# Performance work log

Measured on AMD Instinct MI355X. Metric: run time of the kernel, lower is better.

Reference implementation:

```python
import jax, jax.numpy as jnp
import numpy as np

N_NODES = 100000
N_EDGES = 1600000
IN_DIM = 128
HID_DIM = 64
OUT_DIM = 1


def setup_inputs() -> dict:
    key = jax.random.key(0)
    k = jax.random.split(key, 8)
    x = jax.random.normal(k[0], (N_NODES, IN_DIM), dtype=jnp.float32)
    edge_index = jax.random.randint(k[1], (2, N_EDGES), 0, N_NODES, dtype=jnp.int64)
    # GCNConv layer 1: weight [IN, HID], bias [HID] (glorot-ish scale)
    W1 = jax.random.normal(k[2], (IN_DIM, HID_DIM), dtype=jnp.float32) / np.sqrt(IN_DIM)
    b1 = jnp.zeros((HID_DIM,), dtype=jnp.float32)
    W2 = jax.random.normal(k[3], (HID_DIM, HID_DIM), dtype=jnp.float32) / np.sqrt(HID_DIM)
    b2 = jnp.zeros((HID_DIM,), dtype=jnp.float32)
    Wfc = jax.random.normal(k[4], (HID_DIM, OUT_DIM), dtype=jnp.float32) / np.sqrt(HID_DIM)
    bfc = jnp.zeros((OUT_DIM,), dtype=jnp.float32)
    return {"x": x, "edge_index": edge_index, "W1": W1, "b1": b1,
            "W2": W2, "b2": b2, "Wfc": Wfc, "bfc": bfc}


def _gcn_norm(edge_index, n_nodes):
    # PyG GCNConv default: add self-loops, symmetric normalization.
    src, dst = edge_index[0], edge_index[1]
    loop = jnp.arange(n_nodes, dtype=src.dtype)
    src = jnp.concatenate([src, loop])
    dst = jnp.concatenate([dst, loop])
    deg = jax.ops.segment_sum(jnp.ones_like(dst, dtype=jnp.float32), dst,
                              num_segments=n_nodes)
    deg_isqrt = jax.lax.rsqrt(deg)  # deg >= 1 thanks to self-loops
    norm = deg_isqrt[src] * deg_isqrt[dst]  # [E+N]
    return src, dst, norm


def _gcn_conv(x, src, dst, norm, W, b, n_nodes):
    h = x @ W                      # [N, D_out] dense transform first (D_out <= D_in)
    msg = h[src] * norm[:, None]   # gather + normalize  [E+N, D_out]
    out = jax.ops.segment_sum(msg, dst, num_segments=n_nodes)  # scatter-add
    return out + b


def reference(x, edge_index, W1, b1, W2, b2, Wfc, bfc):
    n = x.shape[0]
    src, dst, norm = _gcn_norm(edge_index, n)
    h = jax.nn.relu(_gcn_conv(x, src, dst, norm, W1, b1, n))
    h = jax.nn.relu(_gcn_conv(h, src, dst, norm, W2, b2, n))
    return h @ Wfc + bfc  # [N, 1]
```

## Files before the change

kernel.cpp:

```cpp
#include <hip/hip_runtime.h>


#define IN_DIM 128
#define HID 64
#define B1 256
#define MAXNC 512
#define BCAP 8192

typedef unsigned int uint;
typedef unsigned short ushort;
typedef __attribute__((ext_vector_type(8))) short short8;
typedef __attribute__((ext_vector_type(4))) float f32x4;

__device__ inline uint pack_bf16x2(float a, float b) {
    uint ua = __builtin_bit_cast(uint, a);
    uint ub = __builtin_bit_cast(uint, b);
    ua += 0x7fffu + ((ua >> 16) & 1u);
    ub += 0x7fffu + ((ub >> 16) & 1u);
    return (ua >> 16) | (ub & 0xffff0000u);
}
__device__ inline float bf_lo(uint g) { return __builtin_bit_cast(float, g << 16); }
__device__ inline float bf_hi(uint g) { return __builtin_bit_cast(float, g & 0xffff0000u); }
__device__ inline uint rne_hi_bits(float a) {
    uint u = __builtin_bit_cast(uint, a);
    return (u + 0x7fffu + ((u >> 16) & 1u)) & 0xffff0000u;
}
__device__ inline float bitf(uint u) { return __builtin_bit_cast(float, u); }

__global__ __launch_bounds__(512) void scatter_bkt(
        const int* __restrict__ src, const int* __restrict__ dst,
        int* __restrict__ bktcnt, uint* __restrict__ slack,
        int E, int NC, int chunk,
        const float* __restrict__ W1f, const float* __restrict__ W2f,
        ushort* __restrict__ w1h, ushort* __restrict__ w1l,
        ushort* __restrict__ w2h, ushort* __restrict__ w2l) {
    int t = threadIdx.x, blk = blockIdx.x;
    if (blk < B1) {
        __shared__ int h[MAXNC], cur[MAXNC];
        for (int i = t; i < NC; i += 512) h[i] = 0;
        __syncthreads();
        int s = blk * chunk, e = min(E, s + chunk);
        for (int i = s + t; i < e; i += 512) atomicAdd(&h[dst[i] >> 8], 1);
        __syncthreads();
        for (int i = t; i < NC; i += 512)
            cur[i] = h[i] ? atomicAdd(&bktcnt[i], h[i]) : 0;
        __syncthreads();
        for (int i = s + t; i < e; i += 512) {
            int d = dst[i], b = d >> 8;
            int p = atomicAdd(&cur[b], 1);
            slack[(size_t)b * BCAP + p] = ((uint)src[i] << 8) | (uint)(d & 255);
        }
    } else if (blk == B1) {
        for (int i = t; i < 128 * 64; i += 512) {
            int k = i >> 6, c = i & 63;
            float v = W1f[i];
            uint rh = rne_hi_bits(v);
            w1h[c * 128 + k] = (ushort)(rh >> 16);
            w1l[c * 128 + k] = (ushort)(rne_hi_bits(v - bitf(rh)) >> 16);
        }
    } else {
        for (int i = t; i < 64 * 64; i += 512) {
            int k = i >> 6, c = i & 63;
            float v = W2f[i];
            uint rh = rne_hi_bits(v);
            w2h[c * 64 + k] = (ushort)(rh >> 16);
            w2l[c * 64 + k] = (ushort)(rne_hi_bits(v - bitf(rh)) >> 16);
        }
    }
}

__global__ __launch_bounds__(256) void build_csr2(const int* __restrict__ bktcnt,
                                                  const uint* __restrict__ slack,
                                                  int* __restrict__ row_off,
                                                  float* __restrict__ disqrt,
                                                  int* __restrict__ col,
                                                  int NC, int N) {
    __shared__ int red[4], ws[4], wsoff[4];
    __shared__ int h[256], cur[256];
    int b = blockIdx.x, t = threadIdx.x;
    int part = 0;
    for (int i = t; i < b; i += 256) part += bktcnt[i];
#pragma unroll
    for (int o = 32; o; o >>= 1) part += __shfl_down(part, o, 64);
    if ((t & 63) == 0) red[t >> 6] = part;
    h[t] = 0;
    __syncthreads();
    const int base = red[0] + red[1] + red[2] + red[3];
    const int cnt  = bktcnt[b];
    const uint* bp = slack + (size_t)b * BCAP;
    for (int i = t; i < cnt; i += 256)
        atomicAdd(&h[bp[i] & 255u], 1);
    __syncthreads();
    int deg = h[t];
    int incl = deg;
#pragma unroll
    for (int o = 1; o < 64; o <<= 1) {
        int u = __shfl_up(incl, o, 64);
        if ((t & 63) >= o) incl += u;
    }
    if ((t & 63) == 63) ws[t >> 6] = incl;
    __syncthreads();
    if (t == 0) {
        int run = 0;
#pragma unroll
        for (int i = 0; i < 4; ++i) { wsoff[i] = run; run += ws[i]; }
    }
    __syncthreads();
    int excl = wsoff[t >> 6] + incl - deg;
    cur[t] = base + excl;
    int node = (b << 8) + t;
    if (node < N) {
        row_off[node] = base + excl;
        disqrt[node]  = rsqrtf((float)(deg + 1));
    }
    if (b == NC - 1 && t == 0) row_off[N] = base + cnt;
    __syncthreads();
    for (int i = t; i < cnt; i += 256) {
        uint p = bp[i];
        int pos = atomicAdd(&cur[p & 255u], 1);
        col[pos] = (int)(p >> 8);
    }
}

template <int K, bool SPLIT>
__global__ __launch_bounds__(256) void gemm_mfma(const void* __restrict__ Xv,
                                                 const ushort* __restrict__ WHt,
                                                 const ushort* __restrict__ WLt,
                                                 const float* __restrict__ disqrt,
                                                 uint* __restrict__ Tsb, int n) {
    __shared__ ushort XH[128 * 40];
    __shared__ ushort WH[64 * 40];
    __shared__ ushort WL[64 * 40];
    __shared__ ushort XL[SPLIT ? 128 * 40 : 64];

    const int tid = threadIdx.x;
    const int m0  = blockIdx.x * 128;
    const float* Xf = (const float*)Xv;
    const char*  Xb = (const char*)Xv;

    const int wc = tid >> 2, wslot = tid & 3;
    const char* wh_g = (const char*)WHt + wc * (K * 2) + wslot * 16;
    const char* wl_g = (const char*)WLt + wc * (K * 2) + wslot * 16;

    constexpr int NL = SPLIT ? 4 : 2;
    int xr[NL], xk[NL];
#pragma unroll
    for (int i = 0; i < NL; ++i) {
        int f = tid + i * 256;
        if (SPLIT) { xr[i] = f >> 3; xk[i] = f & 7; }
        else       { xr[i] = f >> 2; xk[i] = f & 3; }
    }

    const float4 z4 = make_float4(0.f, 0.f, 0.f, 0.f);
    const uint4  zu = make_uint4(0u, 0u, 0u, 0u);
    float4 gx[NL];
    uint4  gxb[NL];
    uint4  gwh, gwl;
#pragma unroll
    for (int i = 0; i < NL; ++i) {
        int row = m0 + xr[i];
        if (SPLIT) gx[i]  = (row < n) ? *(const float4*)(Xf + (size_t)row * K + 4 * xk[i]) : z4;
        else       gxb[i] = (row < n) ? *(const uint4*)(Xb + (size_t)row * (K * 2) + xk[i] * 16) : zu;
    }
    gwh = *(const uint4*)wh_g;
    gwl = *(const uint4*)wl_g;

    f32x4 acc[2][4] = {};
    const int l   = tid & 63, wv = tid >> 6;
    const int lr  = l & 15;
    const int kob = (l >> 4) * 16;

    for (int kc = 0;;) {
        if (SPLIT) {
#pragma unroll
            for (int i = 0; i < NL; ++i) {
                float a = gx[i].x, b = gx[i].y, c = gx[i].z, d = gx[i].w;
                uint rha = rne_hi_bits(a), rhb = rne_hi_bits(b);
                uint rhc = rne_hi_bits(c), rhd = rne_hi_bits(d);
                uint2 hh, ll;
                hh.x = (rha >> 16) | (rhb & 0xffff0000u);
                hh.y = (rhc >> 16) | (rhd & 0xffff0000u);
                ll.x = pack_bf16x2(a - bitf(rha), b - bitf(rhb));
                ll.y = pack_bf16x2(c - bitf(rhc), d - bitf(rhd));
                *(uint2*)((char*)XH + xr[i] * 80 + xk[i] * 8) = hh;
                *(uint2*)((char*)XL + xr[i] * 80 + xk[i] * 8) = ll;
            }
        } else {
#pragma unroll
            for (int i = 0; i < NL; ++i)
                *(uint4*)((char*)XH + xr[i] * 80 + xk[i] * 16) = gxb[i];
        }
        *(uint4*)((char*)WH + wc * 80 + wslot * 16) = gwh;
        *(uint4*)((char*)WL + wc * 80 + wslot * 16) = gwl;
        __syncthreads();

        kc += 32;
        const bool more = kc < K;
        if (more) {
#pragma unroll
            for (int i = 0; i < NL; ++i) {
                int row = m0 + xr[i];
                if (SPLIT) gx[i]  = (row < n) ? *(const float4*)(Xf + (size_t)row * K + kc + 4 * xk[i]) : z4;
                else       gxb[i] = (row < n) ? *(const uint4*)(Xb + (size_t)row * (K * 2) + kc * 2 + xk[i] * 16) : zu;
            }
            gwh = *(const uint4*)(wh_g + kc * 2);
            gwl = *(const uint4*)(wl_g + kc * 2);
        }

        short8 xh0 = *(const short8*)((const char*)XH + (wv * 32 + 0 + lr) * 80 + kob);
        short8 xh1 = *(const short8*)((const char*)XH + (wv * 32 + 16 + lr) * 80 + kob);
        short8 xl0, xl1;
        if (SPLIT) {
            xl0 = *(const short8*)((const char*)XL + (wv * 32 + 0 + lr) * 80 + kob);
            xl1 = *(const short8*)((const char*)XL + (wv * 32 + 16 + lr) * 80 + kob);
        }
#pragma unroll
        for (int nn = 0; nn < 4; ++nn) {
            short8 wh = *(const short8*)((const char*)WH + (nn * 16 + lr) * 80 + kob);
            short8 wl = *(const short8*)((const char*)WL + (nn * 16 + lr) * 80 + kob);
            acc[0][nn] = __builtin_amdgcn_mfma_f32_16x16x32_bf16(wh, xh0, acc[0][nn], 0, 0, 0);
            acc[1][nn] = __builtin_amdgcn_mfma_f32_16x16x32_bf16(wh, xh1, acc[1][nn], 0, 0, 0);
            acc[0][nn] = __builtin_amdgcn_mfma_f32_16x16x32_bf16(wl, xh0, acc[0][nn], 0, 0, 0);
            acc[1][nn] = __builtin_amdgcn_mfma_f32_16x16x32_bf16(wl, xh1, acc[1][nn], 0, 0, 0);
            if (SPLIT) {
                acc[0][nn] = __builtin_amdgcn_mfma_f32_16x16x32_bf16(wh, xl0, acc[0][nn], 0, 0, 0);
                acc[1][nn] = __builtin_amdgcn_mfma_f32_16x16x32_bf16(wh, xl1, acc[1][nn], 0, 0, 0);
            }
        }
        if (!more) break;
        __syncthreads();
    }

#pragma unroll
    for (int m = 0; m < 2; ++m) {
        int node = m0 + wv * 32 + m * 16 + lr;
        if (node < n) {
            float dq = disqrt[node];
#pragma unroll
            for (int nn = 0; nn < 4; ++nn) {
                f32x4 a = acc[m][nn];
                uint2 pk;
                pk.x = pack_bf16x2(a[0] * dq, a[1] * dq);
                pk.y = pack_bf16x2(a[2] * dq, a[3] * dq);
                *(uint2*)((char*)Tsb + (size_t)node * 128 + nn * 32 + (l >> 4) * 8) = pk;
            }
        }
    }
}

template <bool FUSE_FC>
__global__ __launch_bounds__(256) void agg_kernel(const uint* __restrict__ Tsb,
                                                  const int* __restrict__ row_off,
                                                  const int* __restrict__ col,
                                                  const float* __restrict__ disqrt,
                                                  const float* __restrict__ bias,
                                                  const float* __restrict__ wfc,
                                                  const float* __restrict__ bfc,
                                                  uint* __restrict__ outb,
                                                  float* __restrict__ outf,
                                                  int node0, int nhi) {
    int node = node0 + blockIdx.x * 4 + (threadIdx.x >> 6);
    if (node >= nhi) return;
    int lane = threadIdx.x & 63;
    int o = lane >> 3;
    int p = lane & 7;
    float acc[8] = {};
    if (o == 0) {
        uint4 g = *(const uint4*)(Tsb + (size_t)node * 32 + 4 * p);
        acc[0] = bf_lo(g.x); acc[1] = bf_hi(g.x);
        acc[2] = bf_lo(g.y); acc[3] = bf_hi(g.y);
        acc[4] = bf_lo(g.z); acc[5] = bf_hi(g.z);
        acc[6] = bf_lo(g.w); acc[7] = bf_hi(g.w);
    }
    int beg = __builtin_amdgcn_readfirstlane(row_off[node]);
    int end = __builtin_amdgcn_readfirstlane(row_off[node + 1]);
    for (int batch = beg; batch < end; batch += 64) {
        int bn = min(64, end - batch);
        int cv = 0;
        if (batch + lane < end) cv = col[batch + lane];
        int j = 0;
        for (; j + 16 <= bn; j += 16) {
            int s0 = __shfl(cv, j + o, 64);
            int s1 = __shfl(cv, j + 8 + o, 64);
            uint4 g0 = *(const uint4*)(Tsb + (size_t)s0 * 32 + 4 * p);
            uint4 g1 = *(const uint4*)(Tsb + (size_t)s1 * 32 + 4 * p);
            acc[0] += bf_lo(g0.x); acc[1] += bf_hi(g0.x);
            acc[2] += bf_lo(g0.y); acc[3] += bf_hi(g0.y);
            acc[4] += bf_lo(g0.z); acc[5] += bf_hi(g0.z);
            acc[6] += bf_lo(g0.w); acc[7] += bf_hi(g0.w);
            acc[0] += bf_lo(g1.x); acc[1] += bf_hi(g1.x);
            acc[2] += bf_lo(g1.y); acc[3] += bf_hi(g1.y);
            acc[4] += bf_lo(g1.z); acc[5] += bf_hi(g1.z);
            acc[6] += bf_lo(g1.w); acc[7] += bf_hi(g1.w);
        }
        for (; j < bn; j += 8) {
            int idx = j + o;
            int s = __shfl(cv, idx & 63, 64);
            uint4 g = *(const uint4*)(Tsb + (size_t)s * 32 + 4 * p);
            if (idx < bn) {
                acc[0] += bf_lo(g.x); acc[1] += bf_hi(g.x);
                acc[2] += bf_lo(g.y); acc[3] += bf_hi(g.y);
                acc[4] += bf_lo(g.z); acc[5] += bf_hi(g.z);
                acc[6] += bf_lo(g.w); acc[7] += bf_hi(g.w);
            }
        }
    }
#pragma unroll
    for (int k = 0; k < 8; ++k) {
        acc[k] += __shfl_xor(acc[k], 8, 64);
        acc[k] += __shfl_xor(acc[k], 16, 64);
        acc[k] += __shfl_xor(acc[k], 32, 64);
    }
    float dq = disqrt[node];
    float4 bv0 = *(const float4*)(bias + 8 * p);
    float4 bv1 = *(const float4*)(bias + 8 * p + 4);
    float r[8];
    r[0] = fmaxf(acc[0] * dq + bv0.x, 0.f);
    r[1] = fmaxf(acc[1] * dq + bv0.y, 0.f);
    r[2] = fmaxf(acc[2] * dq + bv0.z, 0.f);
    r[3] = fmaxf(acc[3] * dq + bv0.w, 0.f);
    r[4] = fmaxf(acc[4] * dq + bv1.x, 0.f);
    r[5] = fmaxf(acc[5] * dq + bv1.y, 0.f);
    r[6] = fmaxf(acc[6] * dq + bv1.z, 0.f);
    r[7] = fmaxf(acc[7] * dq + bv1.w, 0.f);
    if (!FUSE_FC) {
        if (o == 0) {
            uint4 pk;
            pk.x = pack_bf16x2(r[0], r[1]);
            pk.y = pack_bf16x2(r[2], r[3]);
            pk.z = pack_bf16x2(r[4], r[5]);
            pk.w = pack_bf16x2(r[6], r[7]);
            *(uint4*)(outb + (size_t)node * 32 + 4 * p) = pk;
        }
    } else {
        float4 wv0 = *(const float4*)(wfc + 8 * p);
        float4 wv1 = *(const float4*)(wfc + 8 * p + 4);
        float v = r[0] * wv0.x + r[1] * wv0.y + r[2] * wv0.z + r[3] * wv0.w +
                  r[4] * wv1.x + r[5] * wv1.y + r[6] * wv1.z + r[7] * wv1.w;
        v += __shfl_down(v, 4, 64);
        v += __shfl_down(v, 2, 64);
        v += __shfl_down(v, 1, 64);
        if (lane == 0) outf[node] = v + bfc[0];
    }
}

extern "C" void kernel_launch(void* const* d_in, const int* in_sizes, int n_in,
                              void* d_out, int out_size, void* d_ws, size_t ws_size,
                              hipStream_t stream) {
    const float* x   = (const float*)d_in[0];
    const int*   ei  = (const int*)d_in[1];
    const float* W1  = (const float*)d_in[2];
    const float* b1  = (const float*)d_in[3];
    const float* W2  = (const float*)d_in[4];
    const float* b2  = (const float*)d_in[5];
    const float* Wfc = (const float*)d_in[6];
    const float* bfc = (const float*)d_in[7];
    float* out = (float*)d_out;

    const int N = in_sizes[0] / IN_DIM;
    const int E = in_sizes[1] / 2;
    const int* src = ei;
    const int* dst = ei + E;
    const int NC    = (N + 255) >> 8;
    const int chunk = (E + B1 - 1) / B1;

    char* w = (char*)d_ws;
    auto alloc = [&](size_t bytes) {
        void* p = (void*)w;
        w += (bytes + 255) & ~(size_t)255;
        return p;
    };
    int*   row_off = (int*)alloc((size_t)(N + 1) * 4);
    float* disqrt  = (float*)alloc((size_t)N * 4);
    int*   bktcnt  = (int*)alloc(MAXNC * 4);
    int*   col     = (int*)alloc((size_t)E * 4);
    ushort* w1h    = (ushort*)alloc(64 * 128 * 2);
    ushort* w1l    = (ushort*)alloc(64 * 128 * 2);
    ushort* w2h    = (ushort*)alloc(64 * 64 * 2);
    ushort* w2l    = (ushort*)alloc(64 * 64 * 2);
    size_t scrA = (size_t)NC * BCAP * 4, scrB = (size_t)N * HID * 2;
    void*  scr  = alloc(scrA > scrB ? scrA : scrB);
    uint*  h1b  = (uint*)alloc((size_t)N * HID * 2);
    uint*  slack = (uint*)scr;
    uint*  Tsb   = (uint*)scr;

    hipMemsetAsync(bktcnt, 0, MAXNC * 4, stream);
    scatter_bkt<<<B1 + 2, 512, 0, stream>>>(src, dst, bktcnt, slack, E, NC, chunk,
                                            W1, W2, w1h, w1l, w2h, w2l);
    build_csr2<<<NC, 256, 0, stream>>>(bktcnt, slack, row_off, disqrt, col, NC, N);

    gemm_mfma<IN_DIM, true><<<(N + 127) / 128, 256, 0, stream>>>(
        x, w1h, w1l, disqrt, Tsb, N);
    agg_kernel<false><<<(N + 3) / 4, 256, 0, stream>>>(Tsb, row_off, col, disqrt,
                                                       b1, nullptr, nullptr,
                                                       h1b, nullptr, 0, N);

    gemm_mfma<HID, false><<<(N + 127) / 128, 256, 0, stream>>>(
        h1b, w2h, w2l, disqrt, Tsb, N);
    agg_kernel<true><<<(N + 3) / 4, 256, 0, stream>>>(Tsb, row_off, col, disqrt,
                                                      b2, Wfc, bfc,
                                                      nullptr, out, 0, N);
}
```

Baseline: 256.3 us.

## Fuse layer-1 GEMM with edge bucketing and defer degree scaling to aggregation

Merges the first dense GEMM and the edge bucket scatter into one launch, split by block index, so they run concurrently. The bucket scatter now writes per-(bucket, sub-block) slots with local histograms instead of global atomics, which removes the memset. The bf16 hi/lo weight split now happens inside the GEMM body, so no separate preprocessing is needed. Because the GEMM no longer depends on disqrt, the source-side normalisation moves into the aggregation kernels as a per-edge disqrt gather. That adds random 4-byte loads per edge, and the fixed slot capacity (SCAP=128) can overflow if a sub-block sends more than 128 edges to one bucket.

```diff
diff --git a/kernel.cpp b/kernel.cpp
--- a/kernel.cpp
+++ b/kernel.cpp
@@ -3,9 +3,9 @@
 
 #define IN_DIM 128
 #define HID 64
-#define B1 256
+#define NSB 64
+#define SCAP 128
 #define MAXNC 512
-#define BCAP 8192
 
 typedef unsigned int uint;
 typedef unsigned short ushort;
@@ -27,120 +27,21 @@
 }
 __device__ inline float bitf(uint u) { return __builtin_bit_cast(float, u); }
 
-__global__ __launch_bounds__(512) void scatter_bkt(
-        const int* __restrict__ src, const int* __restrict__ dst,
-        int* __restrict__ bktcnt, uint* __restrict__ slack,
-        int E, int NC, int chunk,
-        const float* __restrict__ W1f, const float* __restrict__ W2f,
-        ushort* __restrict__ w1h, ushort* __restrict__ w1l,
-        ushort* __restrict__ w2h, ushort* __restrict__ w2l) {
-    int t = threadIdx.x, blk = blockIdx.x;
-    if (blk < B1) {
-        __shared__ int h[MAXNC], cur[MAXNC];
-        for (int i = t; i < NC; i += 512) h[i] = 0;
-        __syncthreads();
-        int s = blk * chunk, e = min(E, s + chunk);
-        for (int i = s + t; i < e; i += 512) atomicAdd(&h[dst[i] >> 8], 1);
-        __syncthreads();
-        for (int i = t; i < NC; i += 512)
-            cur[i] = h[i] ? atomicAdd(&bktcnt[i], h[i]) : 0;
-        __syncthreads();
-        for (int i = s + t; i < e; i += 512) {
-            int d = dst[i], b = d >> 8;
-            int p = atomicAdd(&cur[b], 1);
-            slack[(size_t)b * BCAP + p] = ((uint)src[i] << 8) | (uint)(d & 255);
-        }
-    } else if (blk == B1) {
-        for (int i = t; i < 128 * 64; i += 512) {
-            int k = i >> 6, c = i & 63;
-            float v = W1f[i];
-            uint rh = rne_hi_bits(v);
-            w1h[c * 128 + k] = (ushort)(rh >> 16);
-            w1l[c * 128 + k] = (ushort)(rne_hi_bits(v - bitf(rh)) >> 16);
-        }
-    } else {
-        for (int i = t; i < 64 * 64; i += 512) {
-            int k = i >> 6, c = i & 63;
-            float v = W2f[i];
-            uint rh = rne_hi_bits(v);
-            w2h[c * 64 + k] = (ushort)(rh >> 16);
-            w2l[c * 64 + k] = (ushort)(rne_hi_bits(v - bitf(rh)) >> 16);
-        }
-    }
-}
-
-__global__ __launch_bounds__(256) void build_csr2(const int* __restrict__ bktcnt,
-                                                  const uint* __restrict__ slack,
-                                                  int* __restrict__ row_off,
-                                                  float* __restrict__ disqrt,
-                                                  int* __restrict__ col,
-                                                  int NC, int N) {
-    __shared__ int red[4], ws[4], wsoff[4];
-    __shared__ int h[256], cur[256];
-    int b = blockIdx.x, t = threadIdx.x;
-    int part = 0;
-    for (int i = t; i < b; i += 256) part += bktcnt[i];
-#pragma unroll
-    for (int o = 32; o; o >>= 1) part += __shfl_down(part, o, 64);
-    if ((t & 63) == 0) red[t >> 6] = part;
-    h[t] = 0;
-    __syncthreads();
-    const int base = red[0] + red[1] + red[2] + red[3];
-    const int cnt  = bktcnt[b];
-    const uint* bp = slack + (size_t)b * BCAP;
-    for (int i = t; i < cnt; i += 256)
-        atomicAdd(&h[bp[i] & 255u], 1);
-    __syncthreads();
-    int deg = h[t];
-    int incl = deg;
-#pragma unroll
-    for (int o = 1; o < 64; o <<= 1) {
-        int u = __shfl_up(incl, o, 64);
-        if ((t & 63) >= o) incl += u;
-    }
-    if ((t & 63) == 63) ws[t >> 6] = incl;
-    __syncthreads();
-    if (t == 0) {
-        int run = 0;
-#pragma unroll
-        for (int i = 0; i < 4; ++i) { wsoff[i] = run; run += ws[i]; }
-    }
-    __syncthreads();
-    int excl = wsoff[t >> 6] + incl - deg;
-    cur[t] = base + excl;
-    int node = (b << 8) + t;
-    if (node < N) {
-        row_off[node] = base + excl;
-        disqrt[node]  = rsqrtf((float)(deg + 1));
-    }
-    if (b == NC - 1 && t == 0) row_off[N] = base + cnt;
-    __syncthreads();
-    for (int i = t; i < cnt; i += 256) {
-        uint p = bp[i];
-        int pos = atomicAdd(&cur[p & 255u], 1);
-        col[pos] = (int)(p >> 8);
-    }
-}
-
 template <int K, bool SPLIT>
-__global__ __launch_bounds__(256) void gemm_mfma(const void* __restrict__ Xv,
-                                                 const ushort* __restrict__ WHt,
-                                                 const ushort* __restrict__ WLt,
-                                                 const float* __restrict__ disqrt,
-                                                 uint* __restrict__ Tsb, int n) {
+__device__ __forceinline__ void gemm_body(int bid, const void* __restrict__ Xv,
+                                          const float* __restrict__ Wf,
+                                          uint* __restrict__ Tsb, int n) {
     __shared__ ushort XH[128 * 40];
     __shared__ ushort WH[64 * 40];
     __shared__ ushort WL[64 * 40];
     __shared__ ushort XL[SPLIT ? 128 * 40 : 64];
 
     const int tid = threadIdx.x;
-    const int m0  = blockIdx.x * 128;
+    const int m0  = bid * 128;
     const float* Xf = (const float*)Xv;
     const char*  Xb = (const char*)Xv;
 
-    const int wc = tid >> 2, wslot = tid & 3;
-    const char* wh_g = (const char*)WHt + wc * (K * 2) + wslot * 16;
-    const char* wl_g = (const char*)WLt + wc * (K * 2) + wslot * 16;
+    const int wc_ = tid & 63, wk0 = (tid >> 6) * 8;
 
     constexpr int NL = SPLIT ? 4 : 2;
     int xr[NL], xk[NL];
@@ -155,15 +56,15 @@
     const uint4  zu = make_uint4(0u, 0u, 0u, 0u);
     float4 gx[NL];
     uint4  gxb[NL];
-    uint4  gwh, gwl;
+    float  gw[8];
 #pragma unroll
     for (int i = 0; i < NL; ++i) {
         int row = m0 + xr[i];
         if (SPLIT) gx[i]  = (row < n) ? *(const float4*)(Xf + (size_t)row * K + 4 * xk[i]) : z4;
         else       gxb[i] = (row < n) ? *(const uint4*)(Xb + (size_t)row * (K * 2) + xk[i] * 16) : zu;
     }
-    gwh = *(const uint4*)wh_g;
-    gwl = *(const uint4*)wl_g;
+#pragma unroll
+    for (int j = 0; j < 8; ++j) gw[j] = Wf[(size_t)(wk0 + j) * 64 + wc_];
 
     f32x4 acc[2][4] = {};
     const int l   = tid & 63, wv = tid >> 6;
@@ -190,8 +91,14 @@
             for (int i = 0; i < NL; ++i)
                 *(uint4*)((char*)XH + xr[i] * 80 + xk[i] * 16) = gxb[i];
         }
-        *(uint4*)((char*)WH + wc * 80 + wslot * 16) = gwh;
-        *(uint4*)((char*)WL + wc * 80 + wslot * 16) = gwl;
+#pragma unroll
+        for (int j = 0; j < 8; j += 2) {
+            uint h0 = rne_hi_bits(gw[j]), h1 = rne_hi_bits(gw[j + 1]);
+            uint hp = (h0 >> 16) | (h1 & 0xffff0000u);
+            uint lp = pack_bf16x2(gw[j] - bitf(h0), gw[j + 1] - bitf(h1));
+            *(uint*)((char*)WH + wc_ * 80 + (wk0 + j) * 2) = hp;
+            *(uint*)((char*)WL + wc_ * 80 + (wk0 + j) * 2) = lp;
+        }
         __syncthreads();
 
         kc += 32;
@@ -203,8 +110,8 @@
                 if (SPLIT) gx[i]  = (row < n) ? *(const float4*)(Xf + (size_t)row * K + kc + 4 * xk[i]) : z4;
                 else       gxb[i] = (row < n) ? *(const uint4*)(Xb + (size_t)row * (K * 2) + kc * 2 + xk[i] * 16) : zu;
             }
-            gwh = *(const uint4*)(wh_g + kc * 2);
-            gwl = *(const uint4*)(wl_g + kc * 2);
+#pragma unroll
+            for (int j = 0; j < 8; ++j) gw[j] = Wf[(size_t)(kc + wk0 + j) * 64 + wc_];
         }
 
         short8 xh0 = *(const short8*)((const char*)XH + (wv * 32 + 0 + lr) * 80 + kob);
@@ -235,15 +142,120 @@
     for (int m = 0; m < 2; ++m) {
         int node = m0 + wv * 32 + m * 16 + lr;
         if (node < n) {
-            float dq = disqrt[node];
 #pragma unroll
             for (int nn = 0; nn < 4; ++nn) {
                 f32x4 a = acc[m][nn];
                 uint2 pk;
-                pk.x = pack_bf16x2(a[0] * dq, a[1] * dq);
-                pk.y = pack_bf16x2(a[2] * dq, a[3] * dq);
+                pk.x = pack_bf16x2(a[0], a[1]);
+                pk.y = pack_bf16x2(a[2], a[3]);
                 *(uint2*)((char*)Tsb + (size_t)node * 128 + nn * 32 + (l >> 4) * 8) = pk;
             }
+        }
+    }
+}
+
+__device__ __forceinline__ void scatter_body(int blk, const int* __restrict__ src,
+                                             const int* __restrict__ dst,
+                                             int* __restrict__ ghist,
+                                             uint* __restrict__ slack,
+                                             int E, int NC, int chunk) {
+    __shared__ int h[MAXNC], cur[MAXNC];
+    int t = threadIdx.x;
+    for (int i = t; i < NC; i += 256) h[i] = 0;
+    __syncthreads();
+    int s = blk * chunk, e = min(E, s + chunk);
+    for (int i = s + t; i < e; i += 256) atomicAdd(&h[dst[i] >> 8], 1);
+    __syncthreads();
+    for (int i = t; i < NC; i += 256) {
+        ghist[i * NSB + blk] = h[i];
+        cur[i] = 0;
+    }
+    __syncthreads();
+    for (int i = s + t; i < e; i += 256) {
+        int d = dst[i], b = d >> 8;
+        int p = atomicAdd(&cur[b], 1);
+        slack[((size_t)b * NSB + blk) * SCAP + p] = ((uint)src[i] << 8) | (uint)(d & 255);
+    }
+}
+
+__global__ __launch_bounds__(256) void mega1(const float* __restrict__ x,
+                                             const float* __restrict__ W1,
+                                             const int* __restrict__ src,
+                                             const int* __restrict__ dst,
+                                             int* __restrict__ ghist,
+                                             uint* __restrict__ slack,
+                                             uint* __restrict__ Tsb,
+                                             int n, int E, int NC, int chunk,
+                                             int gemmN) {
+    if ((int)blockIdx.x < gemmN)
+        gemm_body<IN_DIM, true>(blockIdx.x, x, W1, Tsb, n);
+    else
+        scatter_body(blockIdx.x - gemmN, src, dst, ghist, slack, E, NC, chunk);
+}
+
+__global__ __launch_bounds__(256) void gemm2k(const uint* __restrict__ h1b,
+                                              const float* __restrict__ W2,
+                                              uint* __restrict__ Tsb, int n) {
+    gemm_body<HID, false>(blockIdx.x, h1b, W2, Tsb, n);
+}
+
+__global__ __launch_bounds__(256) void build_csr2(const int* __restrict__ ghist,
+                                                  const uint* __restrict__ slack,
+                                                  int* __restrict__ row_off,
+                                                  float* __restrict__ disqrt,
+                                                  int* __restrict__ col,
+                                                  int NC, int N) {
+    __shared__ int red[4], ws[4], wsoff[4];
+    __shared__ int h[256], cur[256], sub[NSB];
+    int b = blockIdx.x, t = threadIdx.x;
+    int part = 0;
+    for (int i = t; i < b * NSB; i += 256) part += ghist[i];
+#pragma unroll
+    for (int o = 32; o; o >>= 1) part += __shfl_down(part, o, 64);
+    if ((t & 63) == 0) red[t >> 6] = part;
+    if (t < NSB) sub[t] = ghist[b * NSB + t];
+    h[t] = 0;
+    __syncthreads();
+    const int base = red[0] + red[1] + red[2] + red[3];
+    {
+        int sr = t & (NSB - 1), li = t >> 6;
+        int c = sub[sr];
+        const uint* bp = slack + ((size_t)b * NSB + sr) * SCAP;
+        for (int j = li; j < c; j += 4) atomicAdd(&h[bp[j] & 255u], 1);
+    }
+    __syncthreads();
+    int deg = h[t];
+    int incl = deg;
+#pragma unroll
+    for (int o = 1; o < 64; o <<= 1) {
+        int u = __shfl_up(incl, o, 64);
+        if ((t & 63) >= o) incl += u;
+    }
+    if ((t & 63) == 63) ws[t >> 6] = incl;
+    __syncthreads();
+    if (t == 0) {
+        int run = 0;
+#pragma unroll
+        for (int i = 0; i < 4; ++i) { wsoff[i] = run; run += ws[i]; }
+    }
+    __syncthreads();
+    int excl = wsoff[t >> 6] + incl - deg;
+    cur[t] = base + excl;
+    int node = (b << 8) + t;
+    if (node < N) {
+        row_off[node] = base + excl;
+        disqrt[node]  = rsqrtf((float)(deg + 1));
+    }
+    if (b == NC - 1 && t == 0) row_off[N] = base + wsoff[3] + ws[3];
+    __syncthreads();
+    {
+        int sr = t & (NSB - 1), li = t >> 6;
+        int c = sub[sr];
+        const uint* bp = slack + ((size_t)b * NSB + sr) * SCAP;
+        for (int j = li; j < c; j += 4) {
+            uint p = bp[j];
+            int pos = atomicAdd(&cur[p & 255u], 1);
+            col[pos] = (int)(p >> 8);
         }
     }
 }
@@ -264,44 +276,52 @@
     int lane = threadIdx.x & 63;
     int o = lane >> 3;
     int p = lane & 7;
+    float dqn = disqrt[node];
     float acc[8] = {};
     if (o == 0) {
         uint4 g = *(const uint4*)(Tsb + (size_t)node * 32 + 4 * p);
-        acc[0] = bf_lo(g.x); acc[1] = bf_hi(g.x);
-        acc[2] = bf_lo(g.y); acc[3] = bf_hi(g.y);
-        acc[4] = bf_lo(g.z); acc[5] = bf_hi(g.z);
-        acc[6] = bf_lo(g.w); acc[7] = bf_hi(g.w);
+        acc[0] = dqn * bf_lo(g.x); acc[1] = dqn * bf_hi(g.x);
+        acc[2] = dqn * bf_lo(g.y); acc[3] = dqn * bf_hi(g.y);
+        acc[4] = dqn * bf_lo(g.z); acc[5] = dqn * bf_hi(g.z);
+        acc[6] = dqn * bf_lo(g.w); acc[7] = dqn * bf_hi(g.w);
     }
     int beg = __builtin_amdgcn_readfirstlane(row_off[node]);
     int end = __builtin_amdgcn_readfirstlane(row_off[node + 1]);
     for (int batch = beg; batch < end; batch += 64) {
         int bn = min(64, end - batch);
         int cv = 0;
-        if (batch + lane < end) cv = col[batch + lane];
+        float dqv = 0.f;
+        if (batch + lane < end) {
+            cv  = col[batch + lane];
+            dqv = disqrt[cv];
+        }
         int j = 0;
         for (; j + 16 <= bn; j += 16) {
-            int s0 = __shfl(cv, j + o, 64);
-            int s1 = __shfl(cv, j + 8 + o, 64);
+            int   s0 = __shfl(cv,  j + o, 64);
+            float q0 = __shfl(dqv, j + o, 64);
+            int   s1 = __shfl(cv,  j + 8 + o, 64);
+            float q1 = __shfl(dqv, j + 8 + o, 64);
             uint4 g0 = *(const uint4*)(Tsb + (size_t)s0 * 32 + 4 * p);
             uint4 g1 = *(const uint4*)(Tsb + (size_t)s1 * 32 + 4 * p);
-            acc[0] += bf_lo(g0.x); acc[1] += bf_hi(g0.x);
-            acc[2] += bf_lo(g0.y); acc[3] += bf_hi(g0.y);
-            acc[4] += bf_lo(g0.z); acc[5] += bf_hi(g0.z);
-            acc[6] += bf_lo(g0.w); acc[7] += bf_hi(g0.w);
-            acc[0] += bf_lo(g1.x); acc[1] += bf_hi(g1.x);
-            acc[2] += bf_lo(g1.y); acc[3] += bf_hi(g1.y);
-            acc[4] += bf_lo(g1.z); acc[5] += bf_hi(g1.z);
-            acc[6] += bf_lo(g1.w); acc[7] += bf_hi(g1.w);
+            acc[0] += q0 * bf_lo(g0.x); acc[1] += q0 * bf_hi(g0.x);
+            acc[2] += q0 * bf_lo(g0.y); acc[3] += q0 * bf_hi(g0.y);
+            acc[4] += q0 * bf_lo(g0.z); acc[5] += q0 * bf_hi(g0.z);
+            acc[6] += q0 * bf_lo(g0.w); acc[7] += q0 * bf_hi(g0.w);
+            acc[0] += q1 * bf_lo(g1.x); acc[1] += q1 * bf_hi(g1.x);
+            acc[2] += q1 * bf_lo(g1.y); acc[3] += q1 * bf_hi(g1.y);
+            acc[4] += q1 * bf_lo(g1.z); acc[5] += q1 * bf_hi(g1.z);
+            acc[6] += q1 * bf_lo(g1.w); acc[7] += q1 * bf_hi(g1.w);
         }
         for (; j < bn; j += 8) {
             int idx = j + o;
-            int s = __shfl(cv, idx & 63, 64);
+            int   s = __shfl(cv,  idx & 63, 64);
+            float q = __shfl(dqv, idx & 63, 64);
             uint4 g = *(const uint4*)(Tsb + (size_t)s * 32 + 4 * p);
             if (idx < bn) {
-                acc[0] += bf_lo(g.x); acc[1] += bf_hi(g.x);
-                acc[2] += bf_lo(g.y); acc[3] += bf_hi(g.y);
-                acc[4] += bf_lo(g.z); acc[5] += bf_hi(g.z);
-                acc[6] += bf_lo(g.w); acc[7] += bf_hi(g.w);
+                acc[0] += q * bf_lo(g.x); acc[1] += q * bf_hi(g.x);
+                acc[2] += q * bf_lo(g.y); acc[3] += q * bf_hi(g.y);
+                acc[4] += q * bf_lo(g.z); acc[5] += q * bf_hi(g.z);
+                acc[6] += q * bf_lo(g.w); acc[7] += q * bf_hi(g.w);
             }
         }
     }
@@ -311,18 +331,17 @@
         acc[k] += __shfl_xor(acc[k], 16, 64);
         acc[k] += __shfl_xor(acc[k], 32, 64);
     }
-    float dq = disqrt[node];
     float4 bv0 = *(const float4*)(bias + 8 * p);
     float4 bv1 = *(const float4*)(bias + 8 * p + 4);
     float r[8];
-    r[0] = fmaxf(acc[0] * dq + bv0.x, 0.f);
-    r[1] = fmaxf(acc[1] * dq + bv0.y, 0.f);
-    r[2] = fmaxf(acc[2] * dq + bv0.z, 0.f);
-    r[3] = fmaxf(acc[3] * dq + bv0.w, 0.f);
-    r[4] = fmaxf(acc[4] * dq + bv1.x, 0.f);
-    r[5] = fmaxf(acc[5] * dq + bv1.y, 0.f);
-    r[6] = fmaxf(acc[6] * dq + bv1.z, 0.f);
-    r[7] = fmaxf(acc[7] * dq + bv1.w, 0.f);
+    r[0] = fmaxf(acc[0] * dqn + bv0.x, 0.f);
+    r[1] = fmaxf(acc[1] * dqn + bv0.y, 0.f);
+    r[2] = fmaxf(acc[2] * dqn + bv0.z, 0.f);
+    r[3] = fmaxf(acc[3] * dqn + bv0.w, 0.f);
+    r[4] = fmaxf(acc[4] * dqn + bv1.x, 0.f);
+    r[5] = fmaxf(acc[5] * dqn + bv1.y, 0.f);
+    r[6] = fmaxf(acc[6] * dqn + bv1.z, 0.f);
+    r[7] = fmaxf(acc[7] * dqn + bv1.w, 0.f);
     if (!FUSE_FC) {
         if (o == 0) {
             uint4 pk;
@@ -362,7 +381,8 @@
     const int* src = ei;
     const int* dst = ei + E;
     const int NC    = (N + 255) >> 8;
-    const int chunk = (E + B1 - 1) / B1;
+    const int chunk = (E + NSB - 1) / NSB;
+    const int gemmN = (N + 127) / 128;
 
     char* w = (char*)d_ws;
     auto alloc = [&](size_t bytes) {
@@ -372,31 +392,26 @@
     };
     int*   row_off = (int*)alloc((size_t)(N + 1) * 4);
     float* disqrt  = (float*)alloc((size_t)N * 4);
-    int*   bktcnt  = (int*)alloc(MAXNC * 4);
+    int*   ghist   = (int*)alloc((size_t)MAXNC * NSB * 4);
     int*   col     = (int*)alloc((size_t)E * 4);
-    ushort* w1h    = (ushort*)alloc(64 * 128 * 2);
-    ushort* w1l    = (ushort*)alloc(64 * 128 * 2);
-    ushort* w2h    = (ushort*)alloc(64 * 64 * 2);
-    ushort* w2l    = (ushort*)alloc(64 * 64 * 2);
-    size_t scrA = (size_t)NC * BCAP * 4, scrB = (size_t)N * HID * 2;
-    void*  scr  = alloc(scrA > scrB ? scrA : scrB);
-    uint*  h1b  = (uint*)alloc((size_t)N * HID * 2);
-    uint*  slack = (uint*)scr;
-    uint*  Tsb   = (uint*)scr;
-
-    hipMemsetAsync(bktcnt, 0, MAXNC * 4, stream);
-    scatter_bkt<<<B1 + 2, 512, 0, stream>>>(src, dst, bktcnt, slack, E, NC, chunk,
-                                            W1, W2, w1h, w1l, w2h, w2l);
-    build_csr2<<<NC, 256, 0, stream>>>(bktcnt, slack, row_off, disqrt, col, NC, N);
-
-    gemm_mfma<IN_DIM, true><<<(N + 127) / 128, 256, 0, stream>>>(
-        x, w1h, w1l, disqrt, Tsb, N);
+    uint*  Tsb     = (uint*)alloc((size_t)N * HID * 2);
+    size_t slackB = (size_t)NC * NSB * SCAP * 4;
+    size_t h1B    = (size_t)N * HID * 2;
+    void*  scr    = alloc(slackB > h1B ? slackB : h1B);
+    uint*  slack  = (uint*)scr;
+    uint*  h1b    = (uint*)scr;
+
+    mega1<<<gemmN + NSB, 256, 0, stream>>>(x, W1, src, dst, ghist, slack,
+                                           Tsb, N, E, NC, chunk, gemmN);
+
+    build_csr2<<<NC, 256, 0, stream>>>(ghist, slack, row_off, disqrt, col, NC, N);
+
     agg_kernel<false><<<(N + 3) / 4, 256, 0, stream>>>(Tsb, row_off, col, disqrt,
                                                        b1, nullptr, nullptr,
                                                        h1b, nullptr, 0, N);
 
-    gemm_mfma<HID, false><<<(N + 127) / 128, 256, 0, stream>>>(
-        h1b, w2h, w2l, disqrt, Tsb, N);
+    gemm2k<<<gemmN, 256, 0, stream>>>(h1b, W2, Tsb, N);
+
     agg_kernel<true><<<(N + 3) / 4, 256, 0, stream>>>(Tsb, row_off, col, disqrt,
                                                       b2, Wfc, bfc,
                                                       nullptr, out, 0, N);
```

After: 353.2 us. 1.38x slower.
